# Kernel tuning notes

Measured on AMD Instinct MI355X. Metric: run time of the kernel, lower is better.

## Reference

```python
import jax, jax.numpy as jnp
import numpy as np

B, S, N, D = 2, 2048, 16, 64


def setup_inputs() -> dict:
    key = jax.random.key(0)
    kq, kk, kv = jax.random.split(key, 3)
    query = jax.random.normal(kq, (B, S, N, D), dtype=jnp.float32)
    key_t = jax.random.normal(kk, (B, S, N, D), dtype=jnp.float32)
    value = jax.random.normal(kv, (B, S, N, D), dtype=jnp.float32)
    mask = jnp.ones((B, 1, S, S), dtype=jnp.int32)
    return {"query": query, "key": key_t, "value": value, "mask": mask}


def reference(query, key, value, mask):
    d_k = query.shape[-1]
    # [b, n, q, k] attention scores
    scores = jnp.einsum('bqnd,bknd->bnqk', query, key) / jnp.sqrt(jnp.float32(d_k))
    scores = jnp.where(mask == 0, -jnp.inf, scores)
    # NOTE: faithful to the source, softmax is over dim=1 (the HEAD axis),
    # not the key axis. Dropout prob is 0.0 -> identity.
    attn_weights = jax.nn.softmax(scores, axis=1)
    out = jnp.einsum('bnqk,bknd->bnqd', attn_weights, value)
    return out
```

## Files before the change

### kernel.cpp

```cpp
#include <hip/hip_runtime.h>
#include <hip/hip_bf16.h>


#define B_ 2
#define S_ 2048
#define N_ 16
#define D_ 64
#define TQ 32
#define TK 32
#define NT 64

typedef __bf16 bf16x4 __attribute__((ext_vector_type(4)));
typedef __bf16 bf16x8 __attribute__((ext_vector_type(8)));
typedef float  f32x16 __attribute__((ext_vector_type(16)));
typedef unsigned int uint32x4 __attribute__((ext_vector_type(4)));

#define QSCALE 0.18033688011112042f

static __device__ __forceinline__ unsigned int cvt_pk_bf16(float a, float b) {
    unsigned int r;
    asm("v_cvt_pk_bf16_f32 %0, %1, %2" : "=v"(r) : "v"(a), "v"(b));
    return r;
}
static __device__ __forceinline__ void permlane_swap(unsigned int& a, unsigned int& b) {
    asm("v_permlane32_swap_b32 %0, %1" : "+v"(a), "+v"(b));
}

__global__ __launch_bounds__(256) void cvt_qk_pack_kernel(
    const float* __restrict__ Qf, const float* __restrict__ Kf,
    __bf16* __restrict__ QP, __bf16* __restrict__ KP)
{
    const int z = blockIdx.z;
    const float* src = (z < B_) ? Qf : Kf;
    __bf16*      dst = (z < B_) ? QP : KP;
    const float scale = (z < B_) ? QSCALE : 1.0f;
    const int b  = (z < B_) ? z : z - B_;
    const int n  = blockIdx.y;
    const int st = blockIdx.x;
    const int t  = threadIdx.x;
    const int ks   = t >> 6;
    const int lane = t & 63;
    const int lo   = lane & 31;
    const int hi   = lane >> 5;

    const float* p = &src[(((size_t)b * S_ + st * 32 + lo) * N_ + n) * D_ + ks * 16 + hi * 8];
    const float4 a0 = *(const float4*)p;
    const float4 a1 = *(const float4*)(p + 4);
    bf16x8 o;
    o[0] = (__bf16)(a0.x * scale); o[1] = (__bf16)(a0.y * scale);
    o[2] = (__bf16)(a0.z * scale); o[3] = (__bf16)(a0.w * scale);
    o[4] = (__bf16)(a1.x * scale); o[5] = (__bf16)(a1.y * scale);
    o[6] = (__bf16)(a1.z * scale); o[7] = (__bf16)(a1.w * scale);
    *(bf16x8*)&dst[(((size_t)b * N_ + n) * NT + st) * 2048 + (size_t)t * 8] = o;
}

__global__ __launch_bounds__(256) void cvt_v_pack_kernel(
    const float* __restrict__ V, __bf16* __restrict__ VP)
{
    __shared__ __bf16 tile[64][68];
    const int s0 = blockIdx.x * 64;
    const int n  = blockIdx.y;
    const int b  = blockIdx.z;
    const int t  = threadIdx.x;

    {
        const int d4 = (t & 15) * 4;
        const int sr = t >> 4;
        #pragma unroll
        for (int r = 0; r < 4; ++r) {
            const int s = sr + r * 16;
            const float4 v = *(const float4*)&V[(((size_t)b * S_ + s0 + s) * N_ + n) * D_ + d4];
            tile[s][d4 + 0] = (__bf16)v.x;
            tile[s][d4 + 1] = (__bf16)v.y;
            tile[s][d4 + 2] = (__bf16)v.z;
            tile[s][d4 + 3] = (__bf16)v.w;
        }
    }
    __syncthreads();
    {
        const int kstep = t >> 7;
        const int dt    = (t >> 6) & 1;
        const int lane  = t & 63;
        const int lo    = lane & 31;
        const int hi    = lane >> 5;
        #pragma unroll
        for (int kt_sub = 0; kt_sub < 2; ++kt_sub) {
            bf16x8 o;
            #pragma unroll
            for (int j = 0; j < 8; ++j)
                o[j] = tile[kt_sub * 32 + kstep * 16 + hi * 8 + j][dt * 32 + lo];
            const size_t kt = (size_t)(blockIdx.x * 2 + kt_sub);
            *(bf16x8*)&VP[(((size_t)b * N_ + n) * NT + kt) * 2048 + (size_t)t * 8] = o;
        }
    }
}

__global__ __launch_bounds__(256, 4) void pass1_z_kernel(
    const __bf16* __restrict__ QP, const __bf16* __restrict__ KP,
    const int* __restrict__ M, float* __restrict__ Zrt)
{
    __shared__ float tile[4][32][33];

    const int tid  = threadIdx.x;
    const int wv   = tid >> 6;
    const int lane = tid & 63;
    const int lo   = lane & 31;
    const int hi   = lane >> 5;

    const int kt = blockIdx.x * 4 + wv;
    const int qt = blockIdx.y;
    const int b  = blockIdx.z;
    const int k0 = kt * TK;
    const int q0 = qt * TQ;

    const __bf16* Qp = QP + ((size_t)b * N_ * NT + qt) * 2048 + (size_t)lane * 8;
    const __bf16* Kp = KP + ((size_t)b * N_ * NT + kt) * 2048 + (size_t)lane * 8;

    f32x16 zsum = {};
    #pragma unroll 4
    for (int h = 0; h < N_; ++h) {
        const __bf16* Qh = Qp + (size_t)h * NT * 2048;
        const __bf16* Kh = Kp + (size_t)h * NT * 2048;
        bf16x8 qf[4], kf[4];
        #pragma unroll
        for (int ks = 0; ks < 4; ++ks) {
            qf[ks] = *(const bf16x8*)(Qh + ks * 512);
            kf[ks] = *(const bf16x8*)(Kh + ks * 512);
        }
        f32x16 s = {};
        #pragma unroll
        for (int ks = 0; ks < 4; ++ks)
            s = __builtin_amdgcn_mfma_f32_32x32x16_bf16(qf[ks], kf[ks], s, 0, 0, 0);
        #pragma unroll
        for (int r = 0; r < 16; ++r) zsum[r] += __builtin_amdgcn_exp2f(s[r]);
    }

    const size_t mb = (size_t)b * S_ * S_;
    #pragma unroll
    for (int r = 0; r < 16; ++r) {
        const int row = (r & 3) + 8 * (r >> 2) + 4 * hi;
        const int m = M[mb + (size_t)(q0 + row) * S_ + (k0 + lo)];
        tile[wv][row][lo] = m ? __builtin_amdgcn_rcpf(zsum[r]) : __builtin_nanf("");
    }
    #pragma unroll
    for (int r = 0; r < 16; ++r) {
        const int kap = (r & 3) + 8 * (r >> 2) + 4 * hi;
        Zrt[mb + (size_t)(k0 + kap) * S_ + (q0 + lo)] = tile[wv][lo][kap];
    }
}

__global__ __launch_bounds__(256, 4) void pass2_av_kernel(
    const __bf16* __restrict__ QP, const __bf16* __restrict__ KP,
    const __bf16* __restrict__ VP, const float* __restrict__ Zrt,
    float* __restrict__ O)
{
    __shared__ __align__(16) float obuf[4][16 * D_];

    const int tid  = threadIdx.x;
    const int wv   = tid >> 6;
    const int lane = tid & 63;
    const int lo   = lane & 31;
    const int hi   = lane >> 5;

    const int qt = blockIdx.x;
    const int n  = blockIdx.y;
    const int b  = blockIdx.z;
    const int q0 = qt * TQ;

    const __bf16* Qh = QP + (((size_t)b * N_ + n) * NT + qt) * 2048 + (size_t)lane * 8;
    const __bf16* Kh = KP + (((size_t)b * N_ + n) * NT) * 2048 + (size_t)lane * 8;
    const __bf16* Vh = VP + (((size_t)b * N_ + n) * NT) * 2048 + (size_t)lane * 8;
    const float*  Zh = Zrt + (size_t)b * S_ * S_;

    bf16x8 qf[4];
    #pragma unroll
    for (int ks = 0; ks < 4; ++ks)
        qf[ks] = *(const bf16x8*)(Qh + ks * 512);

    f32x16 o0 = {};
    f32x16 o1 = {};

    #pragma unroll 2
    for (int t = 0; t < 16; ++t) {
        const int kt = wv * 16 + t;
        const int k0 = kt * TK;
        const __bf16* Kt = Kh + (size_t)kt * 2048;
        const __bf16* Vt = Vh + (size_t)kt * 2048;

        float zr[16];
        #pragma unroll
        for (int r = 0; r < 16; ++r) {
            const int kap = (r & 3) + 8 * (r >> 2) + 4 * hi;
            zr[r] = Zh[(size_t)(k0 + kap) * S_ + q0 + lo];
        }

        bf16x8 vf[2][2];
        #pragma unroll
        for (int kstep = 0; kstep < 2; ++kstep)
            #pragma unroll
            for (int dt = 0; dt < 2; ++dt)
                vf[kstep][dt] = *(const bf16x8*)(Vt + (kstep * 2 + dt) * 512);

        f32x16 s = {};
        #pragma unroll
        for (int ks = 0; ks < 4; ++ks) {
            bf16x8 kf = *(const bf16x8*)(Kt + ks * 512);
            s = __builtin_amdgcn_mfma_f32_32x32x16_bf16(kf, qf[ks], s, 0, 0, 0);
        }

        float w[16];
        #pragma unroll
        for (int r = 0; r < 16; ++r) w[r] = __builtin_amdgcn_exp2f(s[r]) * zr[r];

        #pragma unroll
        for (int kstep = 0; kstep < 2; ++kstep) {
            const int e = kstep * 8;
            unsigned int d0 = cvt_pk_bf16(w[e + 0], w[e + 1]);
            unsigned int d1 = cvt_pk_bf16(w[e + 2], w[e + 3]);
            unsigned int d2 = cvt_pk_bf16(w[e + 4], w[e + 5]);
            unsigned int d3 = cvt_pk_bf16(w[e + 6], w[e + 7]);
            permlane_swap(d0, d2);
            permlane_swap(d1, d3);
            uint32x4 u; u[0] = d0; u[1] = d1; u[2] = d2; u[3] = d3;
            const bf16x8 pa = __builtin_bit_cast(bf16x8, u);
            o0 = __builtin_amdgcn_mfma_f32_32x32x16_bf16(pa, vf[kstep][0], o0, 0, 0, 0);
            o1 = __builtin_amdgcn_mfma_f32_32x32x16_bf16(pa, vf[kstep][1], o1, 0, 0, 0);
        }
    }

    #pragma unroll
    for (int half = 0; half < 2; ++half) {
        if (half) __syncthreads();
        #pragma unroll
        for (int r8 = 0; r8 < 8; ++r8) {
            const int r  = half * 8 + r8;
            const int lr = (r8 & 3) + 8 * (r8 >> 2) + 4 * hi;
            obuf[wv][lr * D_ + lo]      = o0[r];
            obuf[wv][lr * D_ + 32 + lo] = o1[r];
        }
        __syncthreads();
        const int e0 = tid * 4;
        float a0 = 0.f, a1 = 0.f, a2 = 0.f, a3 = 0.f;
        #pragma unroll
        for (int w = 0; w < 4; ++w) {
            const float4 x = *(const float4*)&obuf[w][e0];
            a0 += x.x; a1 += x.y; a2 += x.z; a3 += x.w;
        }
        const int q = half * 16 + (e0 >> 6);
        const int d = e0 & 63;
        *(float4*)&O[(((size_t)b * N_ + n) * S_ + q0 + q) * (size_t)D_ + d]
            = make_float4(a0, a1, a2, a3);
    }
}

__global__ __launch_bounds__(1024) void sdpa_headsm_kernel(
    const float* __restrict__ Q, const float* __restrict__ K,
    const float* __restrict__ V, const int* __restrict__ M,
    float* __restrict__ O)
{
    __shared__ __align__(16) __bf16 pbuf[N_][TQ][40];

    const int tid  = threadIdx.x;
    const int n    = tid >> 6;
    const int lane = tid & 63;
    const int lo   = lane & 31;
    const int hi   = lane >> 5;

    const int q0 = blockIdx.x * TQ;
    const int b  = blockIdx.y;
    const int kz = blockIdx.z;
    const int FITERS = S_ / TK / 4;

    bf16x8 qf[4];
    {
        const float* qrow = Q + (((size_t)b * S_ + (size_t)(q0 + lo)) * N_ + n) * D_;
        #pragma unroll
        for (int ks = 0; ks < 4; ++ks) {
            const float* p = qrow + ks * 16 + hi * 8;
            float4 a0 = *(const float4*)(p);
            float4 a1 = *(const float4*)(p + 4);
            bf16x8 f;
            f[0] = (__bf16)a0.x; f[1] = (__bf16)a0.y;
            f[2] = (__bf16)a0.z; f[3] = (__bf16)a0.w;
            f[4] = (__bf16)a1.x; f[5] = (__bf16)a1.y;
            f[6] = (__bf16)a1.z; f[7] = (__bf16)a1.w;
            qf[ks] = f;
        }
    }

    f32x16 o0 = {};
    f32x16 o1 = {};

    for (int it = 0; it < FITERS; ++it) {
        const int k0 = (kz * FITERS + it) * TK;

        f32x16 s = {};
        #pragma unroll
        for (int ks = 0; ks < 4; ++ks) {
            const float* krow = K + (((size_t)b * S_ + (size_t)(k0 + lo)) * N_ + n) * D_
                                  + ks * 16 + hi * 8;
            float4 a0 = *(const float4*)(krow);
            float4 a1 = *(const float4*)(krow + 4);
            bf16x8 f;
            f[0] = (__bf16)a0.x; f[1] = (__bf16)a0.y;
            f[2] = (__bf16)a0.z; f[3] = (__bf16)a0.w;
            f[4] = (__bf16)a1.x; f[5] = (__bf16)a1.y;
            f[6] = (__bf16)a1.z; f[7] = (__bf16)a1.w;
            s = __builtin_amdgcn_mfma_f32_32x32x16_bf16(qf[ks], f, s, 0, 0, 0);
        }

        bf16x8 vf[2][2];
        #pragma unroll
        for (int kstep = 0; kstep < 2; ++kstep) {
            #pragma unroll
            for (int dt = 0; dt < 2; ++dt) {
                bf16x8 f;
                #pragma unroll
                for (int j = 0; j < 8; ++j) {
                    const int key = k0 + kstep * 16 + hi * 8 + j;
                    f[j] = (__bf16)V[(((size_t)b * S_ + key) * N_ + n) * D_ + dt * 32 + lo];
                }
                vf[kstep][dt] = f;
            }
        }

        #pragma unroll
        for (int r = 0; r < 16; ++r) {
            const int row = (r & 3) + 8 * (r >> 2) + 4 * hi;
            pbuf[n][row][lo] = (__bf16)__builtin_amdgcn_exp2f(s[r] * QSCALE);
        }

        __syncthreads();

        {
            const int tq = tid >> 5;
            const int tk = tid & 31;
            const int m = M[(size_t)b * S_ * S_ + (size_t)(q0 + tq) * S_ + (k0 + tk)];
            float pv[16];
            float sum = 0.f;
            #pragma unroll
            for (int j = 0; j < 16; ++j) { pv[j] = (float)pbuf[j][tq][tk]; sum += pv[j]; }
            const float rd = m ? (1.0f / sum) : __builtin_nanf("");
            #pragma unroll
            for (int j = 0; j < 16; ++j) pbuf[j][tq][tk] = (__bf16)(pv[j] * rd);
        }

        __syncthreads();

        #pragma unroll
        for (int kstep = 0; kstep < 2; ++kstep) {
            bf16x8 wf = *(const bf16x8*)&pbuf[n][lo][kstep * 16 + hi * 8];
            o0 = __builtin_amdgcn_mfma_f32_32x32x16_bf16(wf, vf[kstep][0], o0, 0, 0, 0);
            o1 = __builtin_amdgcn_mfma_f32_32x32x16_bf16(wf, vf[kstep][1], o1, 0, 0, 0);
        }

        __syncthreads();
    }

    #pragma unroll
    for (int r = 0; r < 16; ++r) {
        const int row = (r & 3) + 8 * (r >> 2) + 4 * hi;
        const size_t base = (((size_t)b * N_ + n) * S_ + (q0 + row)) * (size_t)D_;
        atomicAdd(&O[base + lo],      o0[r]);
        atomicAdd(&O[base + 32 + lo], o1[r]);
    }
}

extern "C" void kernel_launch(void* const* d_in, const int* in_sizes, int n_in,
                              void* d_out, int out_size, void* d_ws, size_t ws_size,
                              hipStream_t stream) {
    const float* Q = (const float*)d_in[0];
    const float* K = (const float*)d_in[1];
    const float* V = (const float*)d_in[2];
    const int*   M = (const int*)d_in[3];
    float* O = (float*)d_out;

    const size_t per  = (size_t)B_ * N_ * NT * 2048;
    const size_t zcnt = (size_t)B_ * S_ * S_;
    const size_t need = 3 * per * sizeof(__bf16) + zcnt * sizeof(float);

    if (ws_size >= need) {
        __bf16* QP = (__bf16*)d_ws;
        __bf16* KP = QP + per;
        __bf16* VP = KP + per;
        float*  Zrt = (float*)(VP + per);
        cvt_qk_pack_kernel<<<dim3(NT, N_, B_ * 2), dim3(256), 0, stream>>>(Q, K, QP, KP);
        cvt_v_pack_kernel<<<dim3(S_ / 64, N_, B_), dim3(256), 0, stream>>>(V, VP);
        pass1_z_kernel<<<dim3(S_ / TK / 4, S_ / TQ, B_), dim3(256), 0, stream>>>(QP, KP, M, Zrt);
        pass2_av_kernel<<<dim3(S_ / TQ, N_, B_), dim3(256), 0, stream>>>(QP, KP, VP, Zrt, O);
    } else {
        hipMemsetAsync(d_out, 0, (size_t)out_size * sizeof(float), stream);
        sdpa_headsm_kernel<<<dim3(S_ / TQ, B_, 4), dim3(1024), 0, stream>>>(Q, K, V, M, O);
    }
}
```

Before: 242.2 us.

## Store Z reciprocals in MFMA-fragment tiled layout and fast-path all-ones mask

Pass 1 now has each wave compute two key tiles and writes the reciprocal head-sum in a tiled layout matching the MFMA accumulator fragment. This replaces the LDS transpose and the strided row writes with contiguous float4 stores, and pass 2 reads Z with four float4 loads instead of sixteen strided scalar loads. The mask is read with coalesced int2 loads and reduced with a wave vote, so the per-element mask lookup only runs when some entry is zero. The cost is more registers per wave (launch bounds lowered to 3 waves per SIMD) and half as many waves in pass 1.

```diff
diff --git a/kernel.cpp b/kernel.cpp
--- a/kernel.cpp
+++ b/kernel.cpp
@@ -95,57 +95,82 @@
     }
 }
 
-__global__ __launch_bounds__(256, 4) void pass1_z_kernel(
+__global__ __launch_bounds__(256, 3) void pass1_z_kernel(
     const __bf16* __restrict__ QP, const __bf16* __restrict__ KP,
     const int* __restrict__ M, float* __restrict__ Zrt)
 {
-    __shared__ float tile[4][32][33];
-
     const int tid  = threadIdx.x;
     const int wv   = tid >> 6;
     const int lane = tid & 63;
     const int lo   = lane & 31;
     const int hi   = lane >> 5;
 
-    const int kt = blockIdx.x * 4 + wv;
-    const int qt = blockIdx.y;
-    const int b  = blockIdx.z;
-    const int k0 = kt * TK;
-    const int q0 = qt * TQ;
+    const int ktA = (blockIdx.x * 4 + wv) * 2;
+    const int qt  = blockIdx.y;
+    const int b   = blockIdx.z;
+    const int k0A = ktA * TK;
+    const int q0  = qt * TQ;
 
     const __bf16* Qp = QP + ((size_t)b * N_ * NT + qt) * 2048 + (size_t)lane * 8;
-    const __bf16* Kp = KP + ((size_t)b * N_ * NT + kt) * 2048 + (size_t)lane * 8;
-
-    f32x16 zsum = {};
-    #pragma unroll 4
+    const __bf16* Kp = KP + ((size_t)b * N_ * NT + ktA) * 2048 + (size_t)lane * 8;
+
+    f32x16 zA = {}, zB = {};
+    #pragma unroll 2
     for (int h = 0; h < N_; ++h) {
         const __bf16* Qh = Qp + (size_t)h * NT * 2048;
         const __bf16* Kh = Kp + (size_t)h * NT * 2048;
-        bf16x8 qf[4], kf[4];
+        bf16x8 qf[4], ka[4], kb[4];
         #pragma unroll
         for (int ks = 0; ks < 4; ++ks) {
             qf[ks] = *(const bf16x8*)(Qh + ks * 512);
-            kf[ks] = *(const bf16x8*)(Kh + ks * 512);
-        }
-        f32x16 s = {};
+            ka[ks] = *(const bf16x8*)(Kh + ks * 512);
+            kb[ks] = *(const bf16x8*)(Kh + 2048 + ks * 512);
+        }
+        f32x16 sA = {}, sB = {};
         #pragma unroll
         for (int ks = 0; ks < 4; ++ks)
-            s = __builtin_amdgcn_mfma_f32_32x32x16_bf16(qf[ks], kf[ks], s, 0, 0, 0);
-        #pragma unroll
-        for (int r = 0; r < 16; ++r) zsum[r] += __builtin_amdgcn_exp2f(s[r]);
+            sA = __builtin_amdgcn_mfma_f32_32x32x16_bf16(ka[ks], qf[ks], sA, 0, 0, 0);
+        #pragma unroll
+        for (int ks = 0; ks < 4; ++ks)
+            sB = __builtin_amdgcn_mfma_f32_32x32x16_bf16(kb[ks], qf[ks], sB, 0, 0, 0);
+        #pragma unroll
+        for (int r = 0; r < 16; ++r) {
+            zA[r] += __builtin_amdgcn_exp2f(sA[r]);
+            zB[r] += __builtin_amdgcn_exp2f(sB[r]);
+        }
     }
 
     const size_t mb = (size_t)b * S_ * S_;
+    int ok = 1;
     #pragma unroll
     for (int r = 0; r < 16; ++r) {
-        const int row = (r & 3) + 8 * (r >> 2) + 4 * hi;
-        const int m = M[mb + (size_t)(q0 + row) * S_ + (k0 + lo)];
-        tile[wv][row][lo] = m ? __builtin_amdgcn_rcpf(zsum[r]) : __builtin_nanf("");
-    }
+        const int2 mm = *(const int2*)&M[mb + (size_t)(q0 + 2 * r + hi) * S_ + k0A + 2 * lo];
+        ok &= (mm.x != 0) & (mm.y != 0);
+    }
+
+    float vA[16], vB[16];
     #pragma unroll
     for (int r = 0; r < 16; ++r) {
-        const int kap = (r & 3) + 8 * (r >> 2) + 4 * hi;
-        Zrt[mb + (size_t)(k0 + kap) * S_ + (q0 + lo)] = tile[wv][lo][kap];
+        vA[r] = __builtin_amdgcn_rcpf(zA[r]);
+        vB[r] = __builtin_amdgcn_rcpf(zB[r]);
+    }
+
+    if (!__all(ok)) {
+        #pragma unroll
+        for (int r = 0; r < 16; ++r) {
+            const int kap = (r & 3) + 8 * (r >> 2) + 4 * hi;
+            const size_t rowb = mb + (size_t)(q0 + lo) * S_ + k0A;
+            if (M[rowb + kap] == 0)      vA[r] = __builtin_nanf("");
+            if (M[rowb + 32 + kap] == 0) vB[r] = __builtin_nanf("");
+        }
+    }
+
+    float* ZA = Zrt + (((size_t)b * NT + ktA) * NT + qt) * 1024 + (size_t)lane * 4;
+    float* ZB = ZA + (size_t)NT * 1024;
+    #pragma unroll
+    for (int c = 0; c < 4; ++c) {
+        *(float4*)(ZA + c * 256) = make_float4(vA[4*c], vA[4*c+1], vA[4*c+2], vA[4*c+3]);
+        *(float4*)(ZB + c * 256) = make_float4(vB[4*c], vB[4*c+1], vB[4*c+2], vB[4*c+3]);
     }
 }
 
@@ -170,7 +195,7 @@
     const __bf16* Qh = QP + (((size_t)b * N_ + n) * NT + qt) * 2048 + (size_t)lane * 8;
     const __bf16* Kh = KP + (((size_t)b * N_ + n) * NT) * 2048 + (size_t)lane * 8;
     const __bf16* Vh = VP + (((size_t)b * N_ + n) * NT) * 2048 + (size_t)lane * 8;
-    const float*  Zh = Zrt + (size_t)b * S_ * S_;
+    const float*  Zh = Zrt + (size_t)b * NT * NT * 1024 + (size_t)lane * 4;
 
     bf16x8 qf[4];
     #pragma unroll
@@ -183,16 +208,16 @@
     #pragma unroll 2
     for (int t = 0; t < 16; ++t) {
         const int kt = wv * 16 + t;
-        const int k0 = kt * TK;
         const __bf16* Kt = Kh + (size_t)kt * 2048;
         const __bf16* Vt = Vh + (size_t)kt * 2048;
-
-        float zr[16];
-        #pragma unroll
-        for (int r = 0; r < 16; ++r) {
-            const int kap = (r & 3) + 8 * (r >> 2) + 4 * hi;
-            zr[r] = Zh[(size_t)(k0 + kap) * S_ + q0 + lo];
-        }
+        const float*  Zt = Zh + ((size_t)kt * NT + qt) * 1024;
+
+        float4 z0 = *(const float4*)(Zt);
+        float4 z1 = *(const float4*)(Zt + 256);
+        float4 z2 = *(const float4*)(Zt + 512);
+        float4 z3 = *(const float4*)(Zt + 768);
+        float zr[16] = { z0.x, z0.y, z0.z, z0.w,  z1.x, z1.y, z1.z, z1.w,
+                         z2.x, z2.y, z2.z, z2.w,  z3.x, z3.y, z3.z, z3.w };
 
         bf16x8 vf[2][2];
         #pragma unroll
@@ -376,7 +401,7 @@
     float* O = (float*)d_out;
 
     const size_t per  = (size_t)B_ * N_ * NT * 2048;
-    const size_t zcnt = (size_t)B_ * S_ * S_;
+    const size_t zcnt = (size_t)B_ * NT * NT * 1024;
     const size_t need = 3 * per * sizeof(__bf16) + zcnt * sizeof(float);
 
     if (ws_size >= need) {
@@ -386,8 +411,8 @@
         float*  Zrt = (float*)(VP + per);
         cvt_qk_pack_kernel<<<dim3(NT, N_, B_ * 2), dim3(256), 0, stream>>>(Q, K, QP, KP);
         cvt_v_pack_kernel<<<dim3(S_ / 64, N_, B_), dim3(256), 0, stream>>>(V, VP);
-        pass1_z_kernel<<<dim3(S_ / TK / 4, S_ / TQ, B_), dim3(256), 0, stream>>>(QP, KP, M, Zrt);
-        pass2_av_kernel<<<dim3(S_ / TQ, N_, B_), dim3(256), 0, stream>>>(QP, KP, VP, Zrt, O);
+        pass1_z_kernel<<<dim3(NT / 8, NT, B_), dim3(256), 0, stream>>>(QP, KP, M, Zrt);
+        pass2_av_kernel<<<dim3(NT, N_, B_), dim3(256), 0, stream>>>(QP, KP, VP, Zrt, O);
     } else {
         hipMemsetAsync(d_out, 0, (size_t)out_size * sizeof(float), stream);
         sdpa_headsm_kernel<<<dim3(S_ / TQ, B_, 4), dim3(1024), 0, stream>>>(Q, K, V, M, O);
```

Measured after the change: 220.4 us. 1.1x faster.

## Store normalizer as packed bf16 fragments and split heads across waves in pass1

Applied to the files above, without the earlier changes.

Pass1 now assigns one key tile per block and splits the 16 heads across its four waves, reducing partial sums through shared memory. The reciprocal normalizer is written as bf16 in an MFMA-fragment-packed layout instead of a transposed fp32 matrix, so pass2 loads it with two vector loads per tile. The mask is checked with vectorized int4 loads and a wave vote, and per-element mask lookups run only when some entry is zero. This halves the normalizer's traffic and makes pass2's scattered scalar loads coalesced, at the cost of bf16 rounding of the normalizer and an added block-level reduction and barrier in pass1.

```diff
diff --git a/kernel.cpp b/kernel.cpp
--- a/kernel.cpp
+++ b/kernel.cpp
@@ -97,9 +97,10 @@
 
 __global__ __launch_bounds__(256, 4) void pass1_z_kernel(
     const __bf16* __restrict__ QP, const __bf16* __restrict__ KP,
-    const int* __restrict__ M, float* __restrict__ Zrt)
+    const int* __restrict__ M, __bf16* __restrict__ Zrb)
 {
-    __shared__ float tile[4][32][33];
+    __shared__ float red[16][4][64];
+    __shared__ int okf[4];
 
     const int tid  = threadIdx.x;
     const int wv   = tid >> 6;
@@ -107,7 +108,7 @@
     const int lo   = lane & 31;
     const int hi   = lane >> 5;
 
-    const int kt = blockIdx.x * 4 + wv;
+    const int kt = blockIdx.x;
     const int qt = blockIdx.y;
     const int b  = blockIdx.z;
     const int k0 = kt * TK;
@@ -116,9 +117,10 @@
     const __bf16* Qp = QP + ((size_t)b * N_ * NT + qt) * 2048 + (size_t)lane * 8;
     const __bf16* Kp = KP + ((size_t)b * N_ * NT + kt) * 2048 + (size_t)lane * 8;
 
-    f32x16 zsum = {};
-    #pragma unroll 4
-    for (int h = 0; h < N_; ++h) {
+    f32x16 z = {};
+    #pragma unroll
+    for (int i = 0; i < 4; ++i) {
+        const int h = wv * 4 + i;
         const __bf16* Qh = Qp + (size_t)h * NT * 2048;
         const __bf16* Kh = Kp + (size_t)h * NT * 2048;
         bf16x8 qf[4], kf[4];
@@ -130,28 +132,53 @@
         f32x16 s = {};
         #pragma unroll
         for (int ks = 0; ks < 4; ++ks)
-            s = __builtin_amdgcn_mfma_f32_32x32x16_bf16(qf[ks], kf[ks], s, 0, 0, 0);
-        #pragma unroll
-        for (int r = 0; r < 16; ++r) zsum[r] += __builtin_amdgcn_exp2f(s[r]);
+            s = __builtin_amdgcn_mfma_f32_32x32x16_bf16(kf[ks], qf[ks], s, 0, 0, 0);
+        #pragma unroll
+        for (int r = 0; r < 16; ++r) z[r] += __builtin_amdgcn_exp2f(s[r]);
     }
 
     const size_t mb = (size_t)b * S_ * S_;
-    #pragma unroll
-    for (int r = 0; r < 16; ++r) {
-        const int row = (r & 3) + 8 * (r >> 2) + 4 * hi;
-        const int m = M[mb + (size_t)(q0 + row) * S_ + (k0 + lo)];
-        tile[wv][row][lo] = m ? __builtin_amdgcn_rcpf(zsum[r]) : __builtin_nanf("");
-    }
-    #pragma unroll
-    for (int r = 0; r < 16; ++r) {
-        const int kap = (r & 3) + 8 * (r >> 2) + 4 * hi;
-        Zrt[mb + (size_t)(k0 + kap) * S_ + (q0 + lo)] = tile[wv][lo][kap];
-    }
+    {
+        const int mrow = tid >> 3;
+        const int mcol = (tid & 7) * 4;
+        const int4 mm = *(const int4*)&M[mb + (size_t)(q0 + mrow) * S_ + k0 + mcol];
+        const int ok = (mm.x != 0) & (mm.y != 0) & (mm.z != 0) & (mm.w != 0);
+        const int wok = __all(ok);
+        if (lane == 0) okf[wv] = wok;
+    }
+
+    #pragma unroll
+    for (int r = 0; r < 16; ++r) red[r][wv][lane] = z[r];
+    __syncthreads();
+
+    float v[4];
+    #pragma unroll
+    for (int i = 0; i < 4; ++i) {
+        const int r = wv * 4 + i;
+        const float sum = (red[r][0][lane] + red[r][1][lane])
+                        + (red[r][2][lane] + red[r][3][lane]);
+        v[i] = __builtin_amdgcn_rcpf(sum);
+    }
+
+    if (!(okf[0] & okf[1] & okf[2] & okf[3])) {
+        #pragma unroll
+        for (int i = 0; i < 4; ++i) {
+            const int kap = i + 8 * wv + 4 * hi;
+            if (M[mb + (size_t)(q0 + lo) * S_ + k0 + kap] == 0)
+                v[i] = __builtin_nanf("");
+        }
+    }
+
+    const unsigned int u0 = cvt_pk_bf16(v[0], v[1]);
+    const unsigned int u1 = cvt_pk_bf16(v[2], v[3]);
+    __bf16* Zt = Zrb + (((size_t)b * NT + kt) * NT + qt) * 1024
+               + (wv >> 1) * 512 + (size_t)lane * 8 + (wv & 1) * 4;
+    *(uint2*)Zt = make_uint2(u0, u1);
 }
 
 __global__ __launch_bounds__(256, 4) void pass2_av_kernel(
     const __bf16* __restrict__ QP, const __bf16* __restrict__ KP,
-    const __bf16* __restrict__ VP, const float* __restrict__ Zrt,
+    const __bf16* __restrict__ VP, const __bf16* __restrict__ Zrb,
     float* __restrict__ O)
 {
     __shared__ __align__(16) float obuf[4][16 * D_];
@@ -170,7 +197,7 @@
     const __bf16* Qh = QP + (((size_t)b * N_ + n) * NT + qt) * 2048 + (size_t)lane * 8;
     const __bf16* Kh = KP + (((size_t)b * N_ + n) * NT) * 2048 + (size_t)lane * 8;
     const __bf16* Vh = VP + (((size_t)b * N_ + n) * NT) * 2048 + (size_t)lane * 8;
-    const float*  Zh = Zrt + (size_t)b * S_ * S_;
+    const __bf16* Zb = Zrb + (size_t)b * NT * NT * 1024 + (size_t)lane * 8;
 
     bf16x8 qf[4];
     #pragma unroll
@@ -183,17 +210,16 @@
     #pragma unroll 2
     for (int t = 0; t < 16; ++t) {
         const int kt = wv * 16 + t;
-        const int k0 = kt * TK;
         const __bf16* Kt = Kh + (size_t)kt * 2048;
         const __bf16* Vt = Vh + (size_t)kt * 2048;
-
-        float zr[16];
-        #pragma unroll
-        for (int r = 0; r < 16; ++r) {
-            const int kap = (r & 3) + 8 * (r >> 2) + 4 * hi;
-            zr[r] = Zh[(size_t)(k0 + kap) * S_ + q0 + lo];
-        }
-
+        const __bf16* Zt = Zb + ((size_t)kt * NT + qt) * 1024;
+
+        const bf16x8 za = *(const bf16x8*)(Zt);
+        const bf16x8 zb = *(const bf16x8*)(Zt + 512);
+
+        bf16x8 kf[4];
+        #pragma unroll
+        for (int ks = 0; ks < 4; ++ks) kf[ks] = *(const bf16x8*)(Kt + ks * 512);
         bf16x8 vf[2][2];
         #pragma unroll
         for (int kstep = 0; kstep < 2; ++kstep)
@@ -203,14 +229,14 @@
 
         f32x16 s = {};
         #pragma unroll
-        for (int ks = 0; ks < 4; ++ks) {
-            bf16x8 kf = *(const bf16x8*)(Kt + ks * 512);
-            s = __builtin_amdgcn_mfma_f32_32x32x16_bf16(kf, qf[ks], s, 0, 0, 0);
-        }
+        for (int ks = 0; ks < 4; ++ks)
+            s = __builtin_amdgcn_mfma_f32_32x32x16_bf16(kf[ks], qf[ks], s, 0, 0, 0);
 
         float w[16];
         #pragma unroll
-        for (int r = 0; r < 16; ++r) w[r] = __builtin_amdgcn_exp2f(s[r]) * zr[r];
+        for (int r = 0; r < 8; ++r)  w[r] = __builtin_amdgcn_exp2f(s[r]) * (float)za[r];
+        #pragma unroll
+        for (int r = 8; r < 16; ++r) w[r] = __builtin_amdgcn_exp2f(s[r]) * (float)zb[r - 8];
 
         #pragma unroll
         for (int kstep = 0; kstep < 2; ++kstep) {
@@ -376,18 +402,18 @@
     float* O = (float*)d_out;
 
     const size_t per  = (size_t)B_ * N_ * NT * 2048;
-    const size_t zcnt = (size_t)B_ * S_ * S_;
-    const size_t need = 3 * per * sizeof(__bf16) + zcnt * sizeof(float);
+    const size_t zcnt = (size_t)B_ * NT * NT * 1024;
+    const size_t need = (3 * per + zcnt) * sizeof(__bf16);
 
     if (ws_size >= need) {
         __bf16* QP = (__bf16*)d_ws;
         __bf16* KP = QP + per;
         __bf16* VP = KP + per;
-        float*  Zrt = (float*)(VP + per);
+        __bf16* Zrb = VP + per;
         cvt_qk_pack_kernel<<<dim3(NT, N_, B_ * 2), dim3(256), 0, stream>>>(Q, K, QP, KP);
         cvt_v_pack_kernel<<<dim3(S_ / 64, N_, B_), dim3(256), 0, stream>>>(V, VP);
-        pass1_z_kernel<<<dim3(S_ / TK / 4, S_ / TQ, B_), dim3(256), 0, stream>>>(QP, KP, M, Zrt);
-        pass2_av_kernel<<<dim3(S_ / TQ, N_, B_), dim3(256), 0, stream>>>(QP, KP, VP, Zrt, O);
+        pass1_z_kernel<<<dim3(NT, NT, B_), dim3(256), 0, stream>>>(QP, KP, M, Zrb);
+        pass2_av_kernel<<<dim3(NT, N_, B_), dim3(256), 0, stream>>>(QP, KP, VP, Zrb, O);
     } else {
         hipMemsetAsync(d_out, 0, (size_t)out_size * sizeof(float), stream);
         sdpa_headsm_kernel<<<dim3(S_ / TQ, B_, 4), dim3(1024), 0, stream>>>(Q, K, V, M, O);
```

New measurement: 235.4 us. -2.8%, faster.
